# Kernel optimization log

Hardware: AMD Instinct MI355X
Metric: run time of the kernel (lower is better)

Reference implementation:

```python
import jax, jax.numpy as jnp
import numpy as np

B, L, D = 4, 4096, 1024


def hippo_freqs(dim):
    n = np.arange(dim, dtype=np.float32)
    f = np.sqrt(2 * n + 1)
    f = f / f.max()
    return np.exp(-f * np.log(10000)).astype(np.float32)


def setup_inputs() -> dict:
    key = jax.random.key(0)
    ks = jax.random.split(key, 8)
    s = 1.0 / np.sqrt(D)
    return {
        "x": jax.random.normal(ks[0], (B, L, D), dtype=jnp.float32),
        "omega": jnp.asarray(hippo_freqs(D)),
        "log_gamma": jax.random.normal(ks[1], (D,), dtype=jnp.float32) - 3.0,
        "dt": jnp.float32(0.1),
        "W_psi": jax.random.uniform(ks[2], (2 * D, D), jnp.float32, -s, s),
        "b_psi": jax.random.uniform(ks[3], (2 * D,), jnp.float32, -s, s),
        "W_phi": jax.random.uniform(ks[4], (2 * D, D), jnp.float32, -s, s),
        "b_phi": jax.random.uniform(ks[5], (2 * D,), jnp.float32, -s, s),
        "W_gate": jax.random.uniform(ks[6], (D, D), jnp.float32, -s, s),
        "b_gate": jax.random.uniform(ks[7], (D,), jnp.float32, -s, s),
    }


def _proj(z):
    # exact_projection: per-channel-axis standardization over last dim (biased var)
    mean = z.mean(axis=-1, keepdims=True)
    var = ((z - mean) ** 2).mean(axis=-1, keepdims=True)
    return (z - mean) / (jnp.sqrt(var) + 1e-6)


def reference(x, omega, log_gamma, dt, W_psi, b_psi, W_phi, b_phi, W_gate, b_gate):
    Bn, Ln, Dn = x.shape
    psi_raw = jnp.einsum("bld,ed->ble", x, W_psi) + b_psi
    phi_raw = jnp.einsum("bld,ed->ble", x, W_phi) + b_phi
    psi = jax.lax.complex(psi_raw[..., :Dn], psi_raw[..., Dn:])
    phi = jax.lax.complex(phi_raw[..., :Dn], phi_raw[..., Dn:])
    gate = jax.nn.sigmoid(jnp.einsum("bld,ed->ble", x, W_gate) + b_gate)
    U = gate.astype(psi.dtype) * psi  # [B,L,D] complex

    dt_abs = jnp.abs(dt)
    lam = jax.lax.complex(-jnp.exp(log_gamma), omega)  # [D]
    t_axis = jnp.arange(Ln, dtype=jnp.float32)
    kernel = jnp.exp(lam[None, :] * t_axis[:, None].astype(lam.dtype) * dt_abs)  # [L,D]

    n_fft = 2 * Ln
    Kf = jnp.fft.fft(kernel, n=n_fft, axis=0)          # [2L,D]
    Uf = jnp.fft.fft(U, n=n_fft, axis=1)               # [B,2L,D]
    H = jnp.fft.ifft(Uf * Kf[None], axis=1)[:, :Ln]    # causal conv, [B,L,D]

    H_proj = jax.lax.complex(_proj(H.real), _proj(H.imag))
    return (H_proj * jnp.conj(phi)).real
```

## Files before the change

### kernel.cpp

```cpp
#include <hip/hip_runtime.h>
#include <hip/hip_bf16.h>
#include <math.h>

#define B_ 4
#define L_ 4096
#define D_ 1024
#define M_ (B_*L_)
#define N_ 5120
#define K_ 1024
#define CHUNKS 128
#define LC 32
#define PL ((long)M_ * D_)

#define WS_NEEDED 211812352ull

typedef __attribute__((ext_vector_type(8))) short bf16x8;
typedef __attribute__((ext_vector_type(4))) float f32x4;

__device__ inline float b2f(short s) {
    unsigned u = ((unsigned)(unsigned short)s) << 16;
    float f; __builtin_memcpy(&f, &u, 4); return f;
}

__device__ inline void cvt4(const float4* __restrict__ src, ushort* __restrict__ dst, long j) {
    float4 v = src[j];
    __hip_bfloat16 a = __float2bfloat16(v.x), b = __float2bfloat16(v.y),
                   c = __float2bfloat16(v.z), d = __float2bfloat16(v.w);
    ushort4 o = { *(ushort*)&a, *(ushort*)&b, *(ushort*)&c, *(ushort*)&d };
    *(ushort4*)(dst + j * 4) = o;
}

__global__ void convert_kernel(const float* __restrict__ x,
                               const float* __restrict__ Wpsi,
                               const float* __restrict__ Wphi,
                               const float* __restrict__ Wgate,
                               ushort* __restrict__ xb,
                               ushort* __restrict__ wb) {
    long i0 = (long)blockIdx.x * blockDim.x + threadIdx.x;
    long stride = (long)gridDim.x * blockDim.x;
    const long nx4 = ((long)M_ * K_) >> 2;
    for (long j = i0; j < nx4; j += stride) cvt4((const float4*)x, xb, j);
    const long nW14 = (2048L * 1024) >> 2, nW34 = (1024L * 1024) >> 2;
    for (long j = i0; j < nW14; j += stride) cvt4((const float4*)Wpsi, wb, j);
    for (long j = i0; j < nW14; j += stride) cvt4((const float4*)Wphi, wb + 2048L * 1024, j);
    for (long j = i0; j < nW34; j += stride) cvt4((const float4*)Wgate, wb + 4096L * 1024, j);
}

#define BM 128
#define BN 128
#define BK 64
__global__ __launch_bounds__(256) void gemm_kernel(const __hip_bfloat16* __restrict__ xb,
                                                   const __hip_bfloat16* __restrict__ wb,
                                                   const float* __restrict__ b_psi,
                                                   const float* __restrict__ b_phi,
                                                   const float* __restrict__ b_gate,
                                                   __hip_bfloat16* __restrict__ raw5) {
    __shared__ __hip_bfloat16 As[BM * BK];
    __shared__ __hip_bfloat16 Bs[BN * BK];

    const int tid  = threadIdx.x;
    const int wave = tid >> 6;
    const int lane = tid & 63;
    const int row16 = lane & 15;
    const int quad  = lane >> 4;
    const int m_blk = blockIdx.x * BM;
    const int n_blk = blockIdx.y * BN;
    const int m_off = (wave >> 1) * 64;
    const int n_off = (wave & 1) * 64;

    const int sub_r = lane >> 3;
    const int ci    = lane & 7;

    f32x4 acc[4][4] = {};

    for (int k0 = 0; k0 < K_; k0 += BK) {
        __syncthreads();
#pragma unroll
        for (int j2 = 0; j2 < 4; j2++) {
            int j  = wave * 4 + j2;
            int r  = j * 8 + sub_r;
            int gc = ci ^ (r & 7);
            const __hip_bfloat16* ga = xb + (long)(m_blk + r) * K_ + k0 + gc * 8;
            const __hip_bfloat16* gb = wb + (long)(n_blk + r) * K_ + k0 + gc * 8;
            __builtin_amdgcn_global_load_lds(
                (const __attribute__((address_space(1))) void*)ga,
                (__attribute__((address_space(3))) void*)((char*)As + j * 1024),
                16, 0, 0);
            __builtin_amdgcn_global_load_lds(
                (const __attribute__((address_space(1))) void*)gb,
                (__attribute__((address_space(3))) void*)((char*)Bs + j * 1024),
                16, 0, 0);
        }
        __syncthreads();

#pragma unroll
        for (int ks = 0; ks < 2; ks++) {
            bf16x8 a[4], b[4];
            int c = ks * 4 + quad;
#pragma unroll
            for (int t = 0; t < 4; t++) {
                int ra = m_off + t * 16 + row16;
                a[t] = *(const bf16x8*)((const char*)As + ra * 128 + ((c ^ (ra & 7)) * 16));
                int rb = n_off + t * 16 + row16;
                b[t] = *(const bf16x8*)((const char*)Bs + rb * 128 + ((c ^ (rb & 7)) * 16));
            }
#pragma unroll
            for (int mi = 0; mi < 4; mi++)
#pragma unroll
                for (int ni = 0; ni < 4; ni++)
                    acc[mi][ni] = __builtin_amdgcn_mfma_f32_16x16x32_bf16(a[mi], b[ni], acc[mi][ni], 0, 0, 0);
        }
    }

#pragma unroll
    for (int mi = 0; mi < 4; mi++) {
#pragma unroll
        for (int ni = 0; ni < 4; ni++) {
            int n = n_blk + n_off + ni * 16 + row16;
            float bias = (n < 2048) ? b_psi[n] : (n < 4096) ? b_phi[n - 2048] : b_gate[n - 4096];
            int g = n >> 10, d = n & 1023;
            __hip_bfloat16* pl = raw5 + (long)g * PL;
#pragma unroll
            for (int r = 0; r < 4; r++) {
                int m = m_blk + m_off + mi * 16 + quad * 4 + r;
                pl[(long)m * D_ + d] = __float2bfloat16(acc[mi][ni][r] + bias);
            }
        }
    }
}

__global__ __launch_bounds__(1024) void scan1_kernel(__hip_bfloat16* raw5,
                                                     const float* __restrict__ omega,
                                                     const float* __restrict__ log_gamma,
                                                     const float* __restrict__ dtp,
                                                     float2* __restrict__ E) {
    const int d = threadIdx.x;
    const int c = blockIdx.x;
    const int b = blockIdx.y;
    const float dt = fabsf(dtp[0]);
    const float decay = expf(-expf(log_gamma[d]) * dt);
    const float ang = omega[d] * dt;
    const float ar = decay * cosf(ang), ai = decay * sinf(ang);

    __hip_bfloat16* Pre = raw5;
    __hip_bfloat16* Pim = raw5 + PL;
    const __hip_bfloat16* Gt = raw5 + 4 * PL;
    long base = (long)(b * L_ + c * LC) * D_ + d;

    float hr = 0.f, hi = 0.f;
    for (int i = 0; i < LC; i++) {
        long idx = base + (long)i * D_;
        float sg = 1.f / (1.f + expf(-__bfloat162float(Gt[idx])));
        float ur = sg * __bfloat162float(Pre[idx]);
        float ui = sg * __bfloat162float(Pim[idx]);
        float nhr = ar * hr - ai * hi + ur;
        float nhi = ar * hi + ai * hr + ui;
        hr = nhr; hi = nhi;
        Pre[idx] = __float2bfloat16(hr);
        Pim[idx] = __float2bfloat16(hi);
    }
    E[((long)c * B_ + b) * D_ + d] = make_float2(hr, hi);
}

__global__ void apow_kernel(const float* __restrict__ omega,
                            const float* __restrict__ log_gamma,
                            const float* __restrict__ dtp,
                            float2* __restrict__ apow) {
    int t = blockIdx.x * blockDim.x + threadIdx.x;
    int i = t >> 10, d = t & 1023;
    float dt = fabsf(dtp[0]);
    float e = expf(-expf(log_gamma[d]) * dt * (float)(i + 1));
    float ang = omega[d] * dt * (float)(i + 1);
    apow[t] = make_float2(e * cosf(ang), e * sinf(ang));
}

__global__ __launch_bounds__(128) void carry_kernel(const float2* __restrict__ E,
                                                    const float* __restrict__ omega,
                                                    const float* __restrict__ log_gamma,
                                                    const float* __restrict__ dtp,
                                                    float2* __restrict__ carry) {
    __shared__ float2 sh[CHUNKS];
    const int c = threadIdx.x;
    const int bd = blockIdx.x;
    const int b = bd >> 10, d = bd & 1023;
    const float dt = fabsf(dtp[0]);
    const float gd = expf(log_gamma[d]);
    const float wd = omega[d];

    float2 v = E[((long)c * B_ + b) * D_ + d];
    sh[c] = v;
    __syncthreads();
#pragma unroll
    for (int s = 1; s < CHUNKS; s <<= 1) {
        float2 prev;
        bool has = (c >= s);
        if (has) prev = sh[c - s];
        __syncthreads();
        if (has) {
            float t = dt * (float)LC * (float)s;
            float dec = expf(-gd * t);
            float ang = wd * t;
            float Ar = dec * cosf(ang), Ai = dec * sinf(ang);
            v.x += Ar * prev.x - Ai * prev.y;
            v.y += Ar * prev.y + Ai * prev.x;
            sh[c] = v;
        }
        __syncthreads();
    }
    float2 outv = (c == 0) ? make_float2(0.f, 0.f) : sh[c - 1];
    carry[((long)c * B_ + b) * D_ + d] = outv;
}

__global__ __launch_bounds__(256) void finish_kernel(const __hip_bfloat16* __restrict__ raw5,
                                                     const float2* __restrict__ carry,
                                                     const float2* __restrict__ apow,
                                                     float* __restrict__ out) {
    const int wv = threadIdx.x >> 6, lane = threadIdx.x & 63;
    const int r = blockIdx.x * 4 + wv;
    const int l = r & (L_ - 1);
    const int b = r >> 12;
    const int c = l >> 5, i = l & 31;
    const int d0 = lane * 16;
    const long base = (long)r * D_ + d0;

    const __hip_bfloat16* Hre = raw5;
    const __hip_bfloat16* Him = raw5 + PL;
    const __hip_bfloat16* Pre = raw5 + 2 * PL;
    const __hip_bfloat16* Pim = raw5 + 3 * PL;
    const float2* cr = carry + ((long)c * B_ + b) * D_ + d0;
    const float2* ap = apow + (long)i * D_ + d0;

    bf16x8 hre[2], him[2];
    hre[0] = *(const bf16x8*)(Hre + base);     hre[1] = *(const bf16x8*)(Hre + base + 8);
    him[0] = *(const bf16x8*)(Him + base);     him[1] = *(const bf16x8*)(Him + base + 8);

    float hr[16], hi[16];
    float s0 = 0.f, s1 = 0.f, s2 = 0.f, s3 = 0.f;
#pragma unroll
    for (int j = 0; j < 16; j++) {
        float2 cv = cr[j];
        float2 av = ap[j];
        float fr = av.x * cv.x - av.y * cv.y;
        float fi = av.x * cv.y + av.y * cv.x;
        float xr = b2f(hre[j >> 3][j & 7]) + fr;
        float xi = b2f(him[j >> 3][j & 7]) + fi;
        hr[j] = xr; hi[j] = xi;
        s0 += xr; s1 += xr * xr; s2 += xi; s3 += xi * xi;
    }
#pragma unroll
    for (int m = 1; m < 64; m <<= 1) {
        s0 += __shfl_xor(s0, m);
        s1 += __shfl_xor(s1, m);
        s2 += __shfl_xor(s2, m);
        s3 += __shfl_xor(s3, m);
    }
    float mean_r = s0 * (1.f / D_);
    float var_r  = s1 * (1.f / D_) - mean_r * mean_r;
    float mean_i = s2 * (1.f / D_);
    float var_i  = s3 * (1.f / D_) - mean_i * mean_i;
    float inv_r = 1.f / (sqrtf(fmaxf(var_r, 0.f)) + 1e-6f);
    float inv_i = 1.f / (sqrtf(fmaxf(var_i, 0.f)) + 1e-6f);

    bf16x8 pre[2], pim[2];
    pre[0] = *(const bf16x8*)(Pre + base);     pre[1] = *(const bf16x8*)(Pre + base + 8);
    pim[0] = *(const bf16x8*)(Pim + base);     pim[1] = *(const bf16x8*)(Pim + base + 8);

    float o[16];
#pragma unroll
    for (int j = 0; j < 16; j++)
        o[j] = (hr[j] - mean_r) * inv_r * b2f(pre[j >> 3][j & 7])
             + (hi[j] - mean_i) * inv_i * b2f(pim[j >> 3][j & 7]);
#pragma unroll
    for (int q = 0; q < 4; q++)
        *(float4*)(out + base + q * 4) = make_float4(o[q*4], o[q*4+1], o[q*4+2], o[q*4+3]);
}

extern "C" void kernel_launch(void* const* d_in, const int* in_sizes, int n_in,
                              void* d_out, int out_size, void* d_ws, size_t ws_size,
                              hipStream_t stream) {
    (void)in_sizes; (void)n_in; (void)out_size;
    if (ws_size < WS_NEEDED) return;

    const float* x         = (const float*)d_in[0];
    const float* omega     = (const float*)d_in[1];
    const float* log_gamma = (const float*)d_in[2];
    const float* dt        = (const float*)d_in[3];
    const float* W_psi     = (const float*)d_in[4];
    const float* b_psi     = (const float*)d_in[5];
    const float* W_phi     = (const float*)d_in[6];
    const float* b_phi     = (const float*)d_in[7];
    const float* W_gate    = (const float*)d_in[8];
    const float* b_gate    = (const float*)d_in[9];

    char* ws = (char*)d_ws;
    __hip_bfloat16* xb   = (__hip_bfloat16*)(ws);
    __hip_bfloat16* wb   = (__hip_bfloat16*)(ws + 33554432);
    __hip_bfloat16* raw5 = (__hip_bfloat16*)(ws + 44040192);
    float2* E     = (float2*)(ws);
    float2* carry = (float2*)(ws + 4194304);
    float2* apow  = (float2*)(ws + 8388608);
    float* out = (float*)d_out;

    convert_kernel<<<2048, 256, 0, stream>>>(x, W_psi, W_phi, W_gate, (ushort*)xb, (ushort*)wb);
    gemm_kernel<<<dim3(M_ / BM, N_ / BN), 256, 0, stream>>>(xb, wb, b_psi, b_phi, b_gate, raw5);
    apow_kernel<<<128, 256, 0, stream>>>(omega, log_gamma, dt, apow);
    scan1_kernel<<<dim3(CHUNKS, B_), 1024, 0, stream>>>(raw5, omega, log_gamma, dt, E);
    carry_kernel<<<B_ * D_, 128, 0, stream>>>(E, omega, log_gamma, dt, carry);
    finish_kernel<<<M_ / 4, 256, 0, stream>>>(raw5, carry, apow, out);
}
```

Baseline: 484.3 us.

## Rewrite projection GEMM as 256x256 double-buffered LDS pipeline with tile swizzle

The bf16 projection GEMM moves from 128x128 tiles with a single LDS buffer to 256x256 tiles, 8 waves and a 128 KB double-buffered LDS. Global-to-LDS loads for later k-steps are interleaved with four MFMA quadrant phases, using explicit waitcnt, barriers and setprio. A block-index swizzle groups tiles for better L2 reuse. The goal is to hide load latency and raise MFMA utilisation, at the cost of heavier register and LDS pressure and fragile hand-placed synchronisation.

```diff
diff --git a/kernel.cpp b/kernel.cpp
--- a/kernel.cpp
+++ b/kernel.cpp
@@ -46,85 +46,133 @@
     for (long j = i0; j < nW34; j += stride) cvt4((const float4*)Wgate, wb + 4096L * 1024, j);
 }
 
-#define BM 128
-#define BN 128
-#define BK 64
-__global__ __launch_bounds__(256) void gemm_kernel(const __hip_bfloat16* __restrict__ xb,
-                                                   const __hip_bfloat16* __restrict__ wb,
-                                                   const float* __restrict__ b_psi,
-                                                   const float* __restrict__ b_phi,
-                                                   const float* __restrict__ b_gate,
-                                                   __hip_bfloat16* __restrict__ raw5) {
-    __shared__ __hip_bfloat16 As[BM * BK];
-    __shared__ __hip_bfloat16 Bs[BN * BK];
-
-    const int tid  = threadIdx.x;
-    const int wave = tid >> 6;
-    const int lane = tid & 63;
+#define BM2 256
+#define BN2 256
+#define BK2 64
+#define NT  (K_ / BK2)
+#define DBUF_BYTES 65536
+
+#define STAGE(gptr, brow, kt, slotoff)                                                       \
+  do {                                                                                       \
+    const __hip_bfloat16* g0_ = (gptr) + (long)((brow) + srow0) * K_ + (kt) * 64 + sgc0 * 8; \
+    const __hip_bfloat16* g1_ = (gptr) + (long)((brow) + srow1) * K_ + (kt) * 64 + sgc1 * 8; \
+    __builtin_amdgcn_global_load_lds((const __attribute__((address_space(1))) void*)g0_,     \
+        (__attribute__((address_space(3))) void*)(smem + (slotoff) + ldst0), 16, 0, 0);      \
+    __builtin_amdgcn_global_load_lds((const __attribute__((address_space(1))) void*)g1_,     \
+        (__attribute__((address_space(3))) void*)(smem + (slotoff) + ldst1), 16, 0, 0);      \
+  } while (0)
+
+#define DSA(db, qm)                                                                 \
+  _Pragma("unroll") for (int i_ = 0; i_ < 4; ++i_) {                                \
+    aA[i_][0] = *(const bf16x8*)((db) + aoff + (qm) * 8192 + i_ * 2048 + ct0);      \
+    aA[i_][1] = *(const bf16x8*)((db) + aoff + (qm) * 8192 + i_ * 2048 + ct1);      \
+  }
+#define DSB(db, qn, s)                                                              \
+  _Pragma("unroll") for (int j_ = 0; j_ < 2; ++j_) {                                \
+    bB[s][j_][0] = *(const bf16x8*)((db) + boff + (qn) * 4096 + j_ * 2048 + ct0);   \
+    bB[s][j_][1] = *(const bf16x8*)((db) + boff + (qn) * 4096 + j_ * 2048 + ct1);   \
+  }
+#define MFMA16(qm, qn, s)                                                                         \
+  _Pragma("unroll") for (int i_ = 0; i_ < 4; ++i_)                                                \
+    _Pragma("unroll") for (int j_ = 0; j_ < 2; ++j_) {                                            \
+      acc[(qm)*4+i_][(qn)*2+j_] = __builtin_amdgcn_mfma_f32_16x16x32_bf16(                        \
+          aA[i_][0], bB[s][j_][0], acc[(qm)*4+i_][(qn)*2+j_], 0, 0, 0);                           \
+      acc[(qm)*4+i_][(qn)*2+j_] = __builtin_amdgcn_mfma_f32_16x16x32_bf16(                        \
+          aA[i_][1], bB[s][j_][1], acc[(qm)*4+i_][(qn)*2+j_], 0, 0, 0);                           \
+    }
+#define BARRIER __builtin_amdgcn_s_barrier()
+#define LGKM0 do { asm volatile("s_waitcnt lgkmcnt(0)" ::: "memory");                             \
+                   __builtin_amdgcn_sched_barrier(0); } while (0)
+
+__global__ __launch_bounds__(512, 2)
+void gemm_kernel(const __hip_bfloat16* __restrict__ xb,
+                 const __hip_bfloat16* __restrict__ wb,
+                 const float* __restrict__ b_psi,
+                 const float* __restrict__ b_phi,
+                 const float* __restrict__ b_gate,
+                 __hip_bfloat16* __restrict__ raw5) {
+    __shared__ __attribute__((aligned(16))) char smem[2 * DBUF_BYTES];
+
+    const int tid   = threadIdx.x;
+    const int wid   = tid >> 6;
+    const int lane  = tid & 63;
     const int row16 = lane & 15;
     const int quad  = lane >> 4;
-    const int m_blk = blockIdx.x * BM;
-    const int n_blk = blockIdx.y * BN;
-    const int m_off = (wave >> 1) * 64;
-    const int n_off = (wave & 1) * 64;
-
-    const int sub_r = lane >> 3;
-    const int ci    = lane & 7;
-
-    f32x4 acc[4][4] = {};
-
-    for (int k0 = 0; k0 < K_; k0 += BK) {
-        __syncthreads();
-#pragma unroll
-        for (int j2 = 0; j2 < 4; j2++) {
-            int j  = wave * 4 + j2;
-            int r  = j * 8 + sub_r;
-            int gc = ci ^ (r & 7);
-            const __hip_bfloat16* ga = xb + (long)(m_blk + r) * K_ + k0 + gc * 8;
-            const __hip_bfloat16* gb = wb + (long)(n_blk + r) * K_ + k0 + gc * 8;
-            __builtin_amdgcn_global_load_lds(
-                (const __attribute__((address_space(1))) void*)ga,
-                (__attribute__((address_space(3))) void*)((char*)As + j * 1024),
-                16, 0, 0);
-            __builtin_amdgcn_global_load_lds(
-                (const __attribute__((address_space(1))) void*)gb,
-                (__attribute__((address_space(3))) void*)((char*)Bs + j * 1024),
-                16, 0, 0);
-        }
-        __syncthreads();
-
-#pragma unroll
-        for (int ks = 0; ks < 2; ks++) {
-            bf16x8 a[4], b[4];
-            int c = ks * 4 + quad;
-#pragma unroll
-            for (int t = 0; t < 4; t++) {
-                int ra = m_off + t * 16 + row16;
-                a[t] = *(const bf16x8*)((const char*)As + ra * 128 + ((c ^ (ra & 7)) * 16));
-                int rb = n_off + t * 16 + row16;
-                b[t] = *(const bf16x8*)((const char*)Bs + rb * 128 + ((c ^ (rb & 7)) * 16));
-            }
-#pragma unroll
-            for (int mi = 0; mi < 4; mi++)
-#pragma unroll
-                for (int ni = 0; ni < 4; ni++)
-                    acc[mi][ni] = __builtin_amdgcn_mfma_f32_16x16x32_bf16(a[mi], b[ni], acc[mi][ni], 0, 0, 0);
-        }
-    }
-
-#pragma unroll
-    for (int mi = 0; mi < 4; mi++) {
-#pragma unroll
-        for (int ni = 0; ni < 4; ni++) {
-            int n = n_blk + n_off + ni * 16 + row16;
+    const int wm    = wid >> 2;
+    const int wn    = wid & 3;
+
+    const int bid = blockIdx.y * 64 + blockIdx.x;
+    const int swz = (bid & 7) * (1280 / 8) + (bid >> 3);
+    const int m_blk = (swz & 63) * BM2;
+    const int n_blk = (swz >> 6) * BN2;
+
+    const int srow0 = tid >> 3;
+    const int srow1 = (512 + tid) >> 3;
+    const int sch   = tid & 7;
+    const int sgc0  = sch ^ (srow0 & 7);
+    const int sgc1  = sch ^ (srow1 & 7);
+    const int ldst0 = (wid * 64) * 16;
+    const int ldst1 = (512 + wid * 64) * 16;
+
+    const int sw   = row16 & 7;
+    const int aoff = wm * 16384 + row16 * 128;
+    const int boff = 32768 + (wn >> 1) * 16384 + ((wn & 1) * 64 + row16) * 128;
+    const int ct0  = ((0 * 4 + quad) ^ sw) * 16;
+    const int ct1  = ((1 * 4 + quad) ^ sw) * 16;
+
+    bf16x8 aA[4][2];
+    bf16x8 bB[2][2][2];
+    f32x4  acc[8][4] = {};
+
+    STAGE(xb, m_blk,       0, 0);
+    STAGE(xb, m_blk + 128, 0, 16384);
+    STAGE(wb, n_blk,       0, 32768);
+    STAGE(wb, n_blk + 128, 0, 32768 + 16384);
+    STAGE(wb, n_blk,       1, DBUF_BYTES + 32768);
+    STAGE(wb, n_blk + 128, 1, DBUF_BYTES + 32768 + 16384);
+    asm volatile("s_waitcnt vmcnt(4)" ::: "memory");
+    BARRIER;
+
+    for (int t = 0; t < NT; ++t) {
+        char* db = smem + (t & 1) * DBUF_BYTES;
+        const int nb = ((t + 1) & 1) * DBUF_BYTES;
+        const int cb = (t & 1) * DBUF_BYTES;
+        DSA(db, 0); DSB(db, 0, 0);
+        if (t + 1 < NT) STAGE(xb, m_blk, t + 1, nb);
+        asm volatile("s_waitcnt lgkmcnt(8)" ::: "memory");
+        BARRIER; LGKM0;
+        __builtin_amdgcn_s_setprio(1); MFMA16(0, 0, 0); __builtin_amdgcn_s_setprio(0);
+        BARRIER;
+        DSB(db, 1, 1);
+        if (t + 1 < NT) STAGE(xb, m_blk + 128, t + 1, nb + 16384);
+        BARRIER; LGKM0;
+        __builtin_amdgcn_s_setprio(1); MFMA16(0, 1, 1); __builtin_amdgcn_s_setprio(0);
+        BARRIER;
+        DSA(db, 1);
+        if (t + 2 < NT) STAGE(wb, n_blk, t + 2, cb + 32768);
+        BARRIER; LGKM0;
+        __builtin_amdgcn_s_setprio(1); MFMA16(1, 1, 1); __builtin_amdgcn_s_setprio(0);
+        BARRIER;
+        if (t + 2 < NT) STAGE(wb, n_blk + 128, t + 2, cb + 32768 + 16384);
+        BARRIER; LGKM0;
+        __builtin_amdgcn_s_setprio(1); MFMA16(1, 0, 0); __builtin_amdgcn_s_setprio(0);
+        if (t < NT - 2) { asm volatile("s_waitcnt vmcnt(4)" ::: "memory"); }
+        else            { asm volatile("s_waitcnt vmcnt(0)" ::: "memory"); }
+        BARRIER;
+    }
+
+#pragma unroll
+    for (int mi = 0; mi < 8; ++mi) {
+        const int mbase = m_blk + wm * 128 + (mi >> 2) * 64 + (mi & 3) * 16 + quad * 4;
+#pragma unroll
+        for (int nj = 0; nj < 4; ++nj) {
+            int n = n_blk + wn * 64 + (nj >> 1) * 32 + (nj & 1) * 16 + row16;
             float bias = (n < 2048) ? b_psi[n] : (n < 4096) ? b_phi[n - 2048] : b_gate[n - 4096];
             int g = n >> 10, d = n & 1023;
             __hip_bfloat16* pl = raw5 + (long)g * PL;
 #pragma unroll
-            for (int r = 0; r < 4; r++) {
-                int m = m_blk + m_off + mi * 16 + quad * 4 + r;
-                pl[(long)m * D_ + d] = __float2bfloat16(acc[mi][ni][r] + bias);
-            }
+            for (int r = 0; r < 4; ++r)
+                pl[(long)(mbase + r) * D_ + d] = __float2bfloat16(acc[mi][nj][r] + bias);
         }
     }
 }
@@ -302,7 +350,7 @@
     float* out = (float*)d_out;
 
     convert_kernel<<<2048, 256, 0, stream>>>(x, W_psi, W_phi, W_gate, (ushort*)xb, (ushort*)wb);
-    gemm_kernel<<<dim3(M_ / BM, N_ / BN), 256, 0, stream>>>(xb, wb, b_psi, b_phi, b_gate, raw5);
+    gemm_kernel<<<dim3(M_ / BM2, N_ / BN2), 512, 0, stream>>>(xb, wb, b_psi, b_phi, b_gate, raw5);
     apow_kernel<<<128, 256, 0, stream>>>(omega, log_gamma, dt, apow);
     scan1_kernel<<<dim3(CHUNKS, B_), 1024, 0, stream>>>(raw5, omega, log_gamma, dt, E);
     carry_kernel<<<B_ * D_, 128, 0, stream>>>(E, omega, log_gamma, dt, carry);
```

Result: faster. 440.2 us (-9.1%).

## Rewrite projection GEMM with 256x256 double-buffered tiles and 32x32 MFMA

Applied to the files above, without the earlier changes.

Replaces the 128x128 single-buffered GEMM with a 512-thread kernel that computes 256x256 output tiles. Each wave uses 32x32x16 bf16 MFMA with register double-buffered operand reads and ping-pong LDS buffers, so the next K tile is fetched while the current one is multiplied. A block-index swizzle is added to improve L2 reuse. The goal is more operand reuse and fewer sync stalls in the dominant projection GEMM. The cost is 128KB of LDS per block, which limits occupancy to one block per CU.

```diff
diff --git a/kernel.cpp b/kernel.cpp
--- a/kernel.cpp
+++ b/kernel.cpp
@@ -16,6 +16,7 @@
 
 typedef __attribute__((ext_vector_type(8))) short bf16x8;
 typedef __attribute__((ext_vector_type(4))) float f32x4;
+typedef __attribute__((ext_vector_type(16))) float f32x16;
 
 __device__ inline float b2f(short s) {
     unsigned u = ((unsigned)(unsigned short)s) << 16;
@@ -46,84 +47,109 @@
     for (long j = i0; j < nW34; j += stride) cvt4((const float4*)Wgate, wb + 4096L * 1024, j);
 }
 
-#define BM 128
-#define BN 128
-#define BK 64
-__global__ __launch_bounds__(256) void gemm_kernel(const __hip_bfloat16* __restrict__ xb,
-                                                   const __hip_bfloat16* __restrict__ wb,
-                                                   const float* __restrict__ b_psi,
-                                                   const float* __restrict__ b_phi,
-                                                   const float* __restrict__ b_gate,
-                                                   __hip_bfloat16* __restrict__ raw5) {
-    __shared__ __hip_bfloat16 As[BM * BK];
-    __shared__ __hip_bfloat16 Bs[BN * BK];
+#define BM2 256
+#define BN2 256
+#define BK2 64
+#define NT  (K_ / BK2)
+#define DBUF_BYTES 65536
+
+#define GLOAD(src, dstoff)                                                                  \
+    __builtin_amdgcn_global_load_lds((const __attribute__((address_space(1))) void*)(src),  \
+        (__attribute__((address_space(3))) void*)(smem + (dstoff)), 16, 0, 0)
+
+#define STAGE_TILE(dboff, kt)                                                               \
+  do {                                                                                      \
+    const __hip_bfloat16* pAt_ = pA + (kt) * 64;                                            \
+    const __hip_bfloat16* pBt_ = pB + (kt) * 64;                                            \
+    _Pragma("unroll") for (int ks_ = 0; ks_ < 4; ++ks_) {                                   \
+      GLOAD(pAt_ + ks_ * 16, (dboff) + sdA + ks_ * 1024);                                   \
+      GLOAD(pBt_ + ks_ * 16, (dboff) + sdB + ks_ * 1024);                                   \
+    }                                                                                       \
+  } while (0)
+
+#define READ6(aX, bX, dboff, ks)                                                            \
+  do {                                                                                      \
+    _Pragma("unroll") for (int i_ = 0; i_ < 4; ++i_)                                        \
+      aX[i_] = *(const bf16x8*)(smem + (dboff) + raA + i_ * 4096 + (ks) * 1024 + l16);      \
+    _Pragma("unroll") for (int j_ = 0; j_ < 2; ++j_)                                        \
+      bX[j_] = *(const bf16x8*)(smem + (dboff) + raB + j_ * 4096 + (ks) * 1024 + l16);      \
+  } while (0)
+
+#define MFMA8(aX, bX)                                                                       \
+  _Pragma("unroll") for (int i_ = 0; i_ < 4; ++i_)                                          \
+    _Pragma("unroll") for (int j_ = 0; j_ < 2; ++j_)                                        \
+      acc[i_][j_] = __builtin_amdgcn_mfma_f32_32x32x16_bf16(aX[i_], bX[j_], acc[i_][j_], 0, 0, 0)
+
+#define BARRIER __builtin_amdgcn_s_barrier()
+#define VM0 asm volatile("s_waitcnt vmcnt(0)" ::: "memory")
+
+__global__ __launch_bounds__(512, 2)
+void gemm_kernel(const __hip_bfloat16* __restrict__ xb,
+                 const __hip_bfloat16* __restrict__ wb,
+                 const float* __restrict__ b_psi,
+                 const float* __restrict__ b_phi,
+                 const float* __restrict__ b_gate,
+                 __hip_bfloat16* __restrict__ raw5) {
+    __shared__ __attribute__((aligned(16))) char smem[2 * DBUF_BYTES];
 
     const int tid  = threadIdx.x;
-    const int wave = tid >> 6;
+    const int wid  = tid >> 6;
     const int lane = tid & 63;
-    const int row16 = lane & 15;
-    const int quad  = lane >> 4;
-    const int m_blk = blockIdx.x * BM;
-    const int n_blk = blockIdx.y * BN;
-    const int m_off = (wave >> 1) * 64;
-    const int n_off = (wave & 1) * 64;
-
-    const int sub_r = lane >> 3;
-    const int ci    = lane & 7;
-
-    f32x4 acc[4][4] = {};
-
-    for (int k0 = 0; k0 < K_; k0 += BK) {
-        __syncthreads();
-#pragma unroll
-        for (int j2 = 0; j2 < 4; j2++) {
-            int j  = wave * 4 + j2;
-            int r  = j * 8 + sub_r;
-            int gc = ci ^ (r & 7);
-            const __hip_bfloat16* ga = xb + (long)(m_blk + r) * K_ + k0 + gc * 8;
-            const __hip_bfloat16* gb = wb + (long)(n_blk + r) * K_ + k0 + gc * 8;
-            __builtin_amdgcn_global_load_lds(
-                (const __attribute__((address_space(1))) void*)ga,
-                (__attribute__((address_space(3))) void*)((char*)As + j * 1024),
-                16, 0, 0);
-            __builtin_amdgcn_global_load_lds(
-                (const __attribute__((address_space(1))) void*)gb,
-                (__attribute__((address_space(3))) void*)((char*)Bs + j * 1024),
-                16, 0, 0);
+    const int r32  = lane & 31;
+    const int hi   = lane >> 5;
+    const int l16  = lane * 16;
+    const int wm   = wid >> 2;
+    const int wn   = wid & 3;
+
+    const int bid = blockIdx.y * 64 + blockIdx.x;
+    const int swz = (bid & 7) * (1280 / 8) + (bid >> 3);
+    const int m_blk = (swz & 63) * BM2;
+    const int n_blk = (swz >> 6) * BN2;
+
+    const __hip_bfloat16* pA = xb + (long)(m_blk + wid * 32 + r32) * K_ + hi * 8;
+    const __hip_bfloat16* pB = wb + (long)(n_blk + wid * 32 + r32) * K_ + hi * 8;
+    const int sdA = wid * 4096;
+    const int sdB = 32768 + wid * 4096;
+
+    const int raA = wm * 16384;
+    const int raB = 32768 + wn * 8192;
+
+    bf16x8 a0[4], b0[2], a1[4], b1[2];
+    f32x16 acc[4][2] = {};
+
+    STAGE_TILE(0, 0);
+    VM0;
+    BARRIER;
+    READ6(a0, b0, 0, 0);
+
+    for (int t = 0; t < NT; ++t) {
+        const int db = (t & 1) * DBUF_BYTES;
+        const int nb = ((t + 1) & 1) * DBUF_BYTES;
+        if (t + 1 < NT) STAGE_TILE(nb, t + 1);
+        READ6(a1, b1, db, 1); MFMA8(a0, b0);
+        READ6(a0, b0, db, 2); MFMA8(a1, b1);
+        READ6(a1, b1, db, 3); MFMA8(a0, b0);
+        MFMA8(a1, b1);
+        if (t + 1 < NT) {
+            VM0;
+            BARRIER;
+            READ6(a0, b0, nb, 0);
         }
-        __syncthreads();
-
-#pragma unroll
-        for (int ks = 0; ks < 2; ks++) {
-            bf16x8 a[4], b[4];
-            int c = ks * 4 + quad;
-#pragma unroll
-            for (int t = 0; t < 4; t++) {
-                int ra = m_off + t * 16 + row16;
-                a[t] = *(const bf16x8*)((const char*)As + ra * 128 + ((c ^ (ra & 7)) * 16));
-                int rb = n_off + t * 16 + row16;
-                b[t] = *(const bf16x8*)((const char*)Bs + rb * 128 + ((c ^ (rb & 7)) * 16));
-            }
-#pragma unroll
-            for (int mi = 0; mi < 4; mi++)
-#pragma unroll
-                for (int ni = 0; ni < 4; ni++)
-                    acc[mi][ni] = __builtin_amdgcn_mfma_f32_16x16x32_bf16(a[mi], b[ni], acc[mi][ni], 0, 0, 0);
-        }
-    }
-
-#pragma unroll
-    for (int mi = 0; mi < 4; mi++) {
-#pragma unroll
-        for (int ni = 0; ni < 4; ni++) {
-            int n = n_blk + n_off + ni * 16 + row16;
+    }
+
+#pragma unroll
+    for (int i = 0; i < 4; ++i) {
+        const int m0 = m_blk + (wm * 4 + i) * 32 + 4 * hi;
+#pragma unroll
+        for (int j = 0; j < 2; ++j) {
+            int n = n_blk + (wn * 2 + j) * 32 + r32;
             float bias = (n < 2048) ? b_psi[n] : (n < 4096) ? b_phi[n - 2048] : b_gate[n - 4096];
             int g = n >> 10, d = n & 1023;
             __hip_bfloat16* pl = raw5 + (long)g * PL;
 #pragma unroll
-            for (int r = 0; r < 4; r++) {
-                int m = m_blk + m_off + mi * 16 + quad * 4 + r;
-                pl[(long)m * D_ + d] = __float2bfloat16(acc[mi][ni][r] + bias);
+            for (int r = 0; r < 16; ++r) {
+                int m = m0 + (r & 3) + 8 * (r >> 2);
+                pl[(long)m * D_ + d] = __float2bfloat16(acc[i][j][r] + bias);
             }
         }
     }
@@ -302,7 +328,7 @@
     float* out = (float*)d_out;
 
     convert_kernel<<<2048, 256, 0, stream>>>(x, W_psi, W_phi, W_gate, (ushort*)xb, (ushort*)wb);
-    gemm_kernel<<<dim3(M_ / BM, N_ / BN), 256, 0, stream>>>(xb, wb, b_psi, b_phi, b_gate, raw5);
+    gemm_kernel<<<dim3(M_ / BM2, N_ / BN2), 512, 0, stream>>>(xb, wb, b_psi, b_phi, b_gate, raw5);
     apow_kernel<<<128, 256, 0, stream>>>(omega, log_gamma, dt, apow);
     scan1_kernel<<<dim3(CHUNKS, B_), 1024, 0, stream>>>(raw5, omega, log_gamma, dt, E);
     carry_kernel<<<B_ * D_, 128, 0, stream>>>(E, omega, log_gamma, dt, carry);
```

New measurement: 505.9 us. 1.04x slower.
